# Kernel tuning notes

Measured on AMD Instinct MI355X. Metric: run time of the kernel, lower is better.

The kernel has to match this reference:

```python
import jax, jax.numpy as jnp
import numpy as np

N, SEQ_LEN, HORIZON, F_IN, EMBED, HIDDEN, LAYERS = 4096, 168, 24, 32, 32, 64, 2
G4 = 4 * HIDDEN
# NOTE: original torch code calls nn.LSTM per-step WITHOUT carrying hidden state,
# so each step's LSTM starts from (h0=0, c0=0): W_hh contributes nothing, only b_hh.

def setup_inputs() -> dict:
    key = jax.random.key(0)
    ks = jax.random.split(key, 12)
    s = 0.1
    return {
        "X": jax.random.normal(ks[0], (N, SEQ_LEN, F_IN), jnp.float32),
        "y": jax.random.normal(ks[1], (N, SEQ_LEN), jnp.float32),
        "Xf": jax.random.normal(ks[2], (N, HORIZON, F_IN), jnp.float32),
        "W_embed": jax.random.normal(ks[3], (EMBED, 1), jnp.float32) * s,
        "b_embed": jax.random.normal(ks[4], (EMBED,), jnp.float32) * s,
        "W_ih": jax.random.normal(ks[5], (LAYERS, G4, EMBED + F_IN), jnp.float32) * s,  # layer1 in-dim == HIDDEN == EMBED+F_IN
        "b_ih": jax.random.normal(ks[6], (LAYERS, G4), jnp.float32) * s,
        "b_hh": jax.random.normal(ks[7], (LAYERS, G4), jnp.float32) * s,
        "W_mu": jax.random.normal(ks[8], (1, HIDDEN), jnp.float32) * s,
        "b_mu": jax.random.normal(ks[9], (1,), jnp.float32) * s,
        "W_sigma": jax.random.normal(ks[10], (1, HIDDEN), jnp.float32) * s,
        "b_sigma": jax.random.normal(ks[11], (1,), jnp.float32) * s,
    }


def reference(X, y, Xf, W_embed, b_embed, W_ih, b_ih, b_hh, W_mu, b_mu, W_sigma, b_sigma):
    num_ts = X.shape[0]
    T = SEQ_LEN + HORIZON
    Xall = jnp.concatenate([X, Xf], axis=1)  # (N, T, F_IN)
    y_pad = jnp.concatenate([y, jnp.zeros((num_ts, HORIZON), y.dtype)], axis=1)  # (N, T)
    use_y = jnp.arange(T) < SEQ_LEN  # teacher-forced region

    def step(carry, inputs):
        x_s, y_s, use = inputs  # (N, F_IN), (N,), scalar bool
        ynext = jnp.where(use, y_s[:, None], carry)  # (N, 1)
        yembed = ynext @ W_embed.T + b_embed  # (N, EMBED)
        h = jnp.concatenate([x_s, yembed], axis=1)  # (N, F_IN+EMBED)
        for l in range(LAYERS):  # single LSTM step from zero state per layer
            gates = h @ W_ih[l].T + b_ih[l] + b_hh[l]  # (N, 4H); torch gate order i,f,g,o
            i_g, f_g, g_g, o_g = jnp.split(gates, 4, axis=1)
            c = jax.nn.sigmoid(i_g) * jnp.tanh(g_g)  # f * c0 term vanishes (c0 = 0)
            h = jax.nn.sigmoid(o_g) * jnp.tanh(c)
        h = jax.nn.relu(h)
        mu = h @ W_mu.T + b_mu  # (N, 1)
        sigma = jax.nn.softplus(h @ W_sigma.T + b_sigma) + 1e-6  # log(1+exp(.)) + eps
        lik = (2.0 * np.pi * sigma ** 2) ** (-0.5) * jnp.exp(-((ynext - mu) ** 2) / (2.0 * sigma ** 2))
        return lik, (lik[:, 0], mu[:, 0], sigma[:, 0])

    carry0 = jnp.zeros((num_ts, 1), X.dtype)
    xs = (jnp.swapaxes(Xall, 0, 1), y_pad.T, use_y)
    _, (lik_t, mu_t, sigma_t) = jax.lax.scan(step, carry0, xs)  # each (T, N)
    ypred = lik_t.T[:, SEQ_LEN - 1: SEQ_LEN + HORIZON - 1]  # (N, HORIZON)
    return ypred, mu_t.T, sigma_t.T
```

## Files before the change

### kernel.cpp

```cpp
#include <hip/hip_runtime.h>
#include <math.h>

#define N_TS 4096
#define SEQ  168
#define HOR  24
#define T_ALL 192
#define F_INP 32
#define HID  64
#define NROW 192
#define NB_B (N_TS / 16)
#define NT_B ((N_TS * SEQ) / 64)
#define L2E  1.44269504089f
#define W16F_L1  6144
#define W16F_L1P 18432

typedef _Float16 half8  __attribute__((ext_vector_type(8)));
typedef _Float16 half4  __attribute__((ext_vector_type(4)));
typedef float    floatx4 __attribute__((ext_vector_type(4)));

__device__ __forceinline__ float fexp(float x)  { return __expf(x); }
__device__ __forceinline__ float ex2(float x)   { return __builtin_amdgcn_exp2f(x); }
__device__ __forceinline__ float frcp(float x)  { return __builtin_amdgcn_rcpf(x); }
__device__ __forceinline__ float softplus_(float x) { return (x > 15.0f) ? x : __logf(1.0f + fexp(x)); }

__device__ __forceinline__ float lstm_h(float ip, float gp, float op) {
    const float Ei = ex2(ip);
    const float Eg = ex2(gp);
    const float cc = (1.0f - Eg) * frcp((1.0f + Ei) * (1.0f + Eg));
    const float Ec = ex2(cc * (-2.0f * L2E));
    const float Eo = ex2(op);
    return (1.0f - Ec) * frcp((1.0f + Ec) * (1.0f + Eo));
}

__device__ __forceinline__ half8 cvt8(const float4 a, const float4 b) {
    half8 v;
    v[0]=(_Float16)a.x; v[1]=(_Float16)a.y; v[2]=(_Float16)a.z; v[3]=(_Float16)a.w;
    v[4]=(_Float16)b.x; v[5]=(_Float16)b.y; v[6]=(_Float16)b.z; v[7]=(_Float16)b.w;
    return v;
}

__global__ __launch_bounds__(256) void prep(
    const float* __restrict__ W_ih, const float* __restrict__ b_ih,
    const float* __restrict__ b_hh,
    const float* __restrict__ W_embed, const float* __restrict__ b_embed,
    _Float16* __restrict__ W16f, float* __restrict__ bsum,
    float* __restrict__ wy1, float* __restrict__ b1c)
{
    const int idx = blockIdx.x * 256 + threadIdx.x;
    for (int i = idx; i < 4 * NROW * 8; i += gridDim.x * 256) {
        const int kp  = i & 7;
        const int row = (i >> 3) % NROW;
        const int kb  = (i >> 3) / NROW;
        const int sr  = (row < 64) ? row : row + 64;
        const float sc = (row >= 64 && row < 128) ? (-2.0f * L2E) : (-L2E);
        W16f[i] = (_Float16)(W_ih[sr * HID + kb * 8 + kp] * sc);
    }
    for (int i = idx; i < 8 * NROW * 8; i += gridDim.x * 256) {
        const int kp  = i & 7;
        const int row = (i >> 3) % NROW;
        const int kb  = (i >> 3) / NROW;
        const int sr  = (row < 64) ? row : row + 64;
        const float sc = (row >= 64 && row < 128) ? (-2.0f * L2E) : (-L2E);
        W16f[W16F_L1 + i] = (_Float16)(W_ih[(256 + sr) * HID + kb * 8 + kp] * sc);
    }
    for (int i = idx; i < 8 * NROW * 8; i += gridDim.x * 256) {
        const int kp  = i & 7;
        const int row = (i >> 3) % NROW;
        const int kb  = (i >> 3) / NROW;
        const int k   = kb * 8 + kp;
        const int kk  = k & 31;
        const int d   = (kk >> 1) & 3;
        const int q   = kk >> 3;
        const int e   = kk & 1;
        const int hid = d * 16 + q * 4 + ((k >> 5) << 1) + e;
        const int sr  = (row < 64) ? row : row + 64;
        const float sc = (row >= 64 && row < 128) ? (-2.0f * L2E) : (-L2E);
        W16f[W16F_L1P + i] = (_Float16)(W_ih[(256 + sr) * HID + hid] * sc);
    }
    for (int i = idx; i < 2 * NROW; i += gridDim.x * 256) {
        const int r = i % NROW;
        const int l = i / NROW;
        const int sr = (r < 64) ? r : r + 64;
        const float sc = (r >= 64 && r < 128) ? (-2.0f * L2E) : (-L2E);
        bsum[i] = (b_ih[l * 256 + sr] + b_hh[l * 256 + sr]) * sc;
    }
    if (idx < NROW) {
        const int sr = (idx < 64) ? idx : idx + 64;
        const float sc = (idx >= 64 && idx < 128) ? (-2.0f * L2E) : (-L2E);
        const float* wrow = W_ih + sr * HID + 32;
        float s1 = 0.f, s2 = 0.f;
        #pragma unroll
        for (int k = 0; k < 32; ++k) {
            s1 = fmaf(wrow[k], W_embed[k], s1);
            s2 = fmaf(wrow[k], b_embed[k], s2);
        }
        wy1[idx] = s1 * sc;
        b1c[idx] = (b_ih[sr] + b_hh[sr] + s2) * sc;
    }
}

__global__ __launch_bounds__(256, 6) void fused(
    const float* __restrict__ X,
    const float* __restrict__ y,
    const float* __restrict__ Xf,
    const float* __restrict__ W_embed,
    const float* __restrict__ b_embed,
    const _Float16* __restrict__ W16f,
    const float* __restrict__ bsum,
    const float* __restrict__ wy1,
    const float* __restrict__ b1c,
    const float* __restrict__ W_mu,
    const float* __restrict__ b_mu,
    const float* __restrict__ W_sigma,
    const float* __restrict__ b_sigma,
    float* __restrict__ out)
{
    __shared__ struct __align__(16) {
        _Float16 slab[16 * 64]; float partm[16][4]; float parts[16][4];
        float wyb[NROW]; float b1cb[NROW];
    } sh;

    const int tid = threadIdx.x;
    float* mu_out = out + (size_t)N_TS * HOR;
    float* sg_out = mu_out + (size_t)N_TS * T_ALL;

    if (blockIdx.x < NB_B) {
        __builtin_amdgcn_s_setprio(1);
        const int w    = tid >> 6;
        const int lane = tid & 63;
        const int quad = lane >> 4;
        const int ln   = lane & 15;
        const int n0   = blockIdx.x * 16;

        if (tid < NROW) {
            sh.wyb[tid]  = wy1[tid];
            sh.b1cb[tid] = b1c[tid];
        }

        half8 B1[3];
        half8 B2[3][2];
        float bias2[3];
        #pragma unroll
        for (int j = 0; j < 3; ++j) {
            const int rt = j * 4 + w;
            B1[j] = *(const half8*)(W16f + ((size_t)quad * NROW + rt * 16 + ln) * 8);
            #pragma unroll
            for (int kt = 0; kt < 2; ++kt)
                B2[j][kt] = *(const half8*)(W16f + W16F_L1 + ((size_t)(kt * 4 + quad) * NROW + rt * 16 + ln) * 8);
            bias2[j] = bsum[NROW + rt * 16 + ln];
        }
        const float wmu = W_mu[w * 16 + ln], wsg = W_sigma[w * 16 + ln];
        const float bmu = b_mu[0], bsg = b_sigma[0];

        const float* xfp = Xf + (size_t)(n0 + ln) * HOR * F_INP + quad * 8;
        float4 xa, xb;
        {
            const float* xp = X + ((size_t)(n0 + ln) * SEQ + (SEQ - 1)) * F_INP + quad * 8;
            xa = *(const float4*)xp;
            xb = *(const float4*)(xp + 4);
        }
        float ycur = y[(size_t)(n0 + ln) * SEQ + (SEQ - 1)];
        __syncthreads();

        #pragma unroll 1
        for (int it = 0; it <= HOR + 1; ++it) {
            if (it > 0) {
                const int k = it - 1;
                const float4 m4 = *(const float4*)sh.partm[ln];
                const float4 s4 = *(const float4*)sh.parts[ln];
                const float mu = (m4.x + m4.y) + (m4.z + m4.w) + bmu;
                const float sg = softplus_((s4.x + s4.y) + (s4.z + s4.w) + bsg) + 1e-6f;
                const float d  = ycur - mu;
                const float is = frcp(sg);
                const float lik = 0.39894228040143267f * is * fexp(-0.5f * d * d * is * is);
                if (k > 0 && w == 0 && quad == 0) {
                    const int nn = n0 + ln;
                    const int t  = SEQ + k - 1;
                    mu_out[(size_t)nn * T_ALL + t] = mu;
                    sg_out[(size_t)nn * T_ALL + t] = sg;
                    if (k < HOR) out[(size_t)nn * HOR + k] = lik;
                }
                ycur = lik;
            }
            if (it > HOR) break;

            const half8 xf0 = cvt8(xa, xb);
            if (it < HOR) {
                xa = *(const float4*)(xfp + it * F_INP);
                xb = *(const float4*)(xfp + it * F_INP + 4);
            }

            floatx4 t0 = *(const floatx4*)(sh.b1cb + 0 * 64 + w * 16 + quad * 4);
            floatx4 t1 = *(const floatx4*)(sh.b1cb + 1 * 64 + w * 16 + quad * 4);
            floatx4 t2 = *(const floatx4*)(sh.b1cb + 2 * 64 + w * 16 + quad * 4);
            t0 = __builtin_amdgcn_mfma_f32_16x16x32_f16(B1[0], xf0, t0, 0, 0, 0);
            t1 = __builtin_amdgcn_mfma_f32_16x16x32_f16(B1[1], xf0, t1, 0, 0, 0);
            t2 = __builtin_amdgcn_mfma_f32_16x16x32_f16(B1[2], xf0, t2, 0, 0, 0);

            const floatx4 wy0  = *(const floatx4*)(sh.wyb + 0 * 64 + w * 16 + quad * 4);
            const floatx4 wy1v = *(const floatx4*)(sh.wyb + 1 * 64 + w * 16 + quad * 4);
            const floatx4 wy2  = *(const floatx4*)(sh.wyb + 2 * 64 + w * 16 + quad * 4);

            half4 h1p;
            #pragma unroll
            for (int r = 0; r < 4; ++r) {
                const float ig = fmaf(ycur, wy0[r],  t0[r]);
                const float gg = fmaf(ycur, wy1v[r], t1[r]);
                const float og = fmaf(ycur, wy2[r],  t2[r]);
                h1p[r] = (_Float16)lstm_h(ig, gg, og);
            }
            {
                const int xblk = (2 * w + (quad >> 1)) ^ (ln & 7);
                *(half4*)(&sh.slab[ln * 64 + xblk * 8 + (quad & 1) * 4]) = h1p;
            }
            __syncthreads();

            const half8 a0 = *(const half8*)(&sh.slab[ln * 64 + ((quad ^ (ln & 7)) << 3)]);
            const half8 a1 = *(const half8*)(&sh.slab[ln * 64 + (((4 + quad) ^ (ln & 7)) << 3)]);
            floatx4 acc[3];
            #pragma unroll
            for (int j = 0; j < 3; ++j) {
                acc[j] = (floatx4){bias2[j], bias2[j], bias2[j], bias2[j]};
                acc[j] = __builtin_amdgcn_mfma_f32_16x16x32_f16(a0, B2[j][0], acc[j], 0, 0, 0);
                acc[j] = __builtin_amdgcn_mfma_f32_16x16x32_f16(a1, B2[j][1], acc[j], 0, 0, 0);
            }

            float pmr[4], psr[4];
            #pragma unroll
            for (int r = 0; r < 4; ++r) {
                const float hh = lstm_h(acc[0][r], acc[1][r], acc[2][r]);
                const float hr = fmaxf(hh, 0.0f);
                pmr[r] = hr * wmu;
                psr[r] = hr * wsg;
            }
            #pragma unroll
            for (int off = 1; off < 16; off <<= 1) {
                #pragma unroll
                for (int r = 0; r < 4; ++r) {
                    pmr[r] += __shfl_xor(pmr[r], off, 64);
                    psr[r] += __shfl_xor(psr[r], off, 64);
                }
            }
            if (ln == 0) {
                #pragma unroll
                for (int r = 0; r < 4; ++r) {
                    sh.partm[quad * 4 + r][w] = pmr[r];
                    sh.parts[quad * 4 + r][w] = psr[r];
                }
            }
            __syncthreads();
        }
        return;
    }

    const int w    = tid >> 6;
    const int lane = tid & 63;
    const int quad = lane >> 4;
    const int ln   = lane & 15;
    const int cid  = (blockIdx.x - NB_B) * 64 + w * 16 + ln;

    half8 xfr;
    {
        const float* xp = X + (size_t)cid * F_INP + quad * 8;
        xfr = cvt8(*(const float4*)xp, *(const float4*)(xp + 4));
    }
    const float yv = y[cid];

    half8 a0, a1;
    {
        const _Float16* bp = W16f + quad * 1536 + ln * 8;
        #pragma unroll
        for (int jt = 0; jt < 4; ++jt) {
            floatx4 ai = *(const floatx4*)(b1c + jt * 16 + quad * 4);
            floatx4 ag = *(const floatx4*)(b1c + 64 + jt * 16 + quad * 4);
            floatx4 ao = *(const floatx4*)(b1c + 128 + jt * 16 + quad * 4);
            ai = __builtin_amdgcn_mfma_f32_16x16x32_f16(*(const half8*)(bp + jt * 128),        xfr, ai, 0, 0, 0);
            ag = __builtin_amdgcn_mfma_f32_16x16x32_f16(*(const half8*)(bp + 512 + jt * 128),  xfr, ag, 0, 0, 0);
            ao = __builtin_amdgcn_mfma_f32_16x16x32_f16(*(const half8*)(bp + 1024 + jt * 128), xfr, ao, 0, 0, 0);
            const floatx4 wyi = *(const floatx4*)(wy1 + jt * 16 + quad * 4);
            const floatx4 wyg = *(const floatx4*)(wy1 + 64 + jt * 16 + quad * 4);
            const floatx4 wyo = *(const floatx4*)(wy1 + 128 + jt * 16 + quad * 4);
            a0[2 * jt + 0] = (_Float16)lstm_h(fmaf(yv, wyi[0], ai[0]),
                                              fmaf(yv, wyg[0], ag[0]),
                                              fmaf(yv, wyo[0], ao[0]));
            a0[2 * jt + 1] = (_Float16)lstm_h(fmaf(yv, wyi[1], ai[1]),
                                              fmaf(yv, wyg[1], ag[1]),
                                              fmaf(yv, wyo[1], ao[1]));
            a1[2 * jt + 0] = (_Float16)lstm_h(fmaf(yv, wyi[2], ai[2]),
                                              fmaf(yv, wyg[2], ag[2]),
                                              fmaf(yv, wyo[2], ao[2]));
            a1[2 * jt + 1] = (_Float16)lstm_h(fmaf(yv, wyi[3], ai[3]),
                                              fmaf(yv, wyg[3], ag[3]),
                                              fmaf(yv, wyo[3], ao[3]));
        }
    }

    float pm = 0.f, ps = 0.f;
    {
        const _Float16* bp = W16f + W16F_L1P + quad * 1536 + ln * 8;
        #pragma unroll
        for (int jt = 0; jt < 4; ++jt) {
            floatx4 ai = *(const floatx4*)(bsum + NROW + jt * 16 + quad * 4);
            floatx4 ag = *(const floatx4*)(bsum + NROW + 64 + jt * 16 + quad * 4);
            floatx4 ao = *(const floatx4*)(bsum + NROW + 128 + jt * 16 + quad * 4);
            ai = __builtin_amdgcn_mfma_f32_16x16x32_f16(*(const half8*)(bp + jt * 128),               a0, ai, 0, 0, 0);
            ai = __builtin_amdgcn_mfma_f32_16x16x32_f16(*(const half8*)(bp + 6144 + jt * 128),        a1, ai, 0, 0, 0);
            ag = __builtin_amdgcn_mfma_f32_16x16x32_f16(*(const half8*)(bp + 512 + jt * 128),         a0, ag, 0, 0, 0);
            ag = __builtin_amdgcn_mfma_f32_16x16x32_f16(*(const half8*)(bp + 6144 + 512 + jt * 128),  a1, ag, 0, 0, 0);
            ao = __builtin_amdgcn_mfma_f32_16x16x32_f16(*(const half8*)(bp + 1024 + jt * 128),        a0, ao, 0, 0, 0);
            ao = __builtin_amdgcn_mfma_f32_16x16x32_f16(*(const half8*)(bp + 6144 + 1024 + jt * 128), a1, ao, 0, 0, 0);
            const floatx4 wm  = *(const floatx4*)(W_mu + jt * 16 + quad * 4);
            const floatx4 ws4 = *(const floatx4*)(W_sigma + jt * 16 + quad * 4);
            #pragma unroll
            for (int r = 0; r < 4; ++r) {
                const float hr = fmaxf(lstm_h(ai[r], ag[r], ao[r]), 0.0f);
                pm = fmaf(hr, wm[r], pm);
                ps = fmaf(hr, ws4[r], ps);
            }
        }
    }
    pm += __shfl_xor(pm, 16, 64); pm += __shfl_xor(pm, 32, 64);
    ps += __shfl_xor(ps, 16, 64); ps += __shfl_xor(ps, 32, 64);

    if (quad == 0) {
        const int n = cid / SEQ;
        const int t = cid - n * SEQ;
        const float mu = pm + b_mu[0];
        const float sg = softplus_(ps + b_sigma[0]) + 1e-6f;
        mu_out[(size_t)n * T_ALL + t] = mu;
        sg_out[(size_t)n * T_ALL + t] = sg;
        if (t == SEQ - 1) {
            const float d  = yv - mu;
            const float is = frcp(sg);
            out[(size_t)n * HOR] = 0.39894228040143267f * is * fexp(-0.5f * d * d * is * is);
        }
    }
}

extern "C" void kernel_launch(void* const* d_in, const int* in_sizes, int n_in,
                              void* d_out, int out_size, void* d_ws, size_t ws_size,
                              hipStream_t stream) {
    const float* X       = (const float*)d_in[0];
    const float* y       = (const float*)d_in[1];
    const float* Xf      = (const float*)d_in[2];
    const float* W_embed = (const float*)d_in[3];
    const float* b_embed = (const float*)d_in[4];
    const float* W_ih    = (const float*)d_in[5];
    const float* b_ih    = (const float*)d_in[6];
    const float* b_hh    = (const float*)d_in[7];
    const float* W_mu    = (const float*)d_in[8];
    const float* b_mu    = (const float*)d_in[9];
    const float* W_sigma = (const float*)d_in[10];
    const float* b_sigma = (const float*)d_in[11];

    float* out = (float*)d_out;
    _Float16*  W16f = (_Float16*)d_ws;
    float*     bsum = (float*)((char*)d_ws + 61440);
    float*     wy1  = (float*)((char*)d_ws + 61440 + 1536);
    float*     b1c  = (float*)((char*)d_ws + 61440 + 1536 + 768);

    prep<<<96, 256, 0, stream>>>(W_ih, b_ih, b_hh, W_embed, b_embed,
                                 W16f, bsum, wy1, b1c);

    fused<<<NB_B + NT_B, 256, 0, stream>>>(
        X, y, Xf, W_embed, b_embed, W16f, bsum, wy1, b1c,
        W_mu, b_mu, W_sigma, b_sigma, out);
}
```

Measured before the change: 275.8 us.

## Use persistent teacher-forced blocks with atomic work queue and LDS-staged weights

The teacher-forced part switches from one short block per 64 timesteps to a fixed pool of 1024 persistent 512-thread blocks. Each block stages the layer weights, biases and head weights into shared memory once, then pulls 16-row units from a global atomic counter. The autoregressive blocks now handle 32 series each, as two 16-series groups in one 512-thread block. This cuts block launch overhead and repeated global weight loads, and balances work dynamically against the long-running recurrent blocks. In exchange it adds one atomic per unit and a counter that the prep kernel must reset, and the larger shared-memory union may lower occupancy.

Result: slower. 1.012 ms (+267.1%).

```diff
diff --git a/kernel.cpp b/kernel.cpp
--- a/kernel.cpp
+++ b/kernel.cpp
@@ -8,8 +8,9 @@
 #define F_INP 32
 #define HID  64
 #define NROW 192
-#define NB_B (N_TS / 16)
-#define NT_B ((N_TS * SEQ) / 64)
+#define NB_B (N_TS / 32)
+#define NT_B 1024
+#define NU   ((N_TS * SEQ) / 16)
 #define L2E  1.44269504089f
 #define W16F_L1  6144
 #define W16F_L1P 18432
@@ -44,9 +45,11 @@
     const float* __restrict__ b_hh,
     const float* __restrict__ W_embed, const float* __restrict__ b_embed,
     _Float16* __restrict__ W16f, float* __restrict__ bsum,
-    float* __restrict__ wy1, float* __restrict__ b1c)
+    float* __restrict__ wy1, float* __restrict__ b1c,
+    int* __restrict__ unit_cnt)
 {
     const int idx = blockIdx.x * 256 + threadIdx.x;
+    if (idx == 0) *unit_cnt = 0;
     for (int i = idx; i < 4 * NROW * 8; i += gridDim.x * 256) {
         const int kp  = i & 7;
         const int row = (i >> 3) % NROW;
@@ -99,7 +102,7 @@
     }
 }
 
-__global__ __launch_bounds__(256, 6) void fused(
+__global__ __launch_bounds__(512, 6) void fused(
     const float* __restrict__ X,
     const float* __restrict__ y,
     const float* __restrict__ Xf,
@@ -113,11 +116,21 @@
     const float* __restrict__ b_mu,
     const float* __restrict__ W_sigma,
     const float* __restrict__ b_sigma,
+    int* __restrict__ unit_cnt,
     float* __restrict__ out)
 {
-    __shared__ struct __align__(16) {
-        _Float16 slab[16 * 64]; float partm[16][4]; float parts[16][4];
-        float wyb[NROW]; float b1cb[NROW];
+    __shared__ union __align__(16) {
+        struct {
+            _Float16 Wl0[6144];
+            _Float16 Wl1[12288];
+            float b1cb[NROW]; float wy1b[NROW]; float bs1b[NROW];
+            float wmb[HID]; float wsb[HID];
+        } P;
+        struct {
+            _Float16 slab[2][1024];
+            float partm[2][16][4]; float parts[2][16][4];
+            float wyb[NROW]; float b1cb[NROW];
+        } B;
     } sh;
 
     const int tid = threadIdx.x;
@@ -127,14 +140,16 @@
     if (blockIdx.x < NB_B) {
         __builtin_amdgcn_s_setprio(1);
         const int w    = tid >> 6;
+        const int g    = w >> 2;
+        const int wg   = w & 3;
         const int lane = tid & 63;
         const int quad = lane >> 4;
         const int ln   = lane & 15;
-        const int n0   = blockIdx.x * 16;
+        const int n0   = blockIdx.x * 32 + g * 16;
 
         if (tid < NROW) {
-            sh.wyb[tid]  = wy1[tid];
-            sh.b1cb[tid] = b1c[tid];
+            sh.B.wyb[tid]  = wy1[tid];
+            sh.B.b1cb[tid] = b1c[tid];
         }
 
         half8 B1[3];
@@ -142,14 +157,14 @@
         float bias2[3];
         #pragma unroll
         for (int j = 0; j < 3; ++j) {
-            const int rt = j * 4 + w;
+            const int rt = j * 4 + wg;
             B1[j] = *(const half8*)(W16f + ((size_t)quad * NROW + rt * 16 + ln) * 8);
             #pragma unroll
             for (int kt = 0; kt < 2; ++kt)
                 B2[j][kt] = *(const half8*)(W16f + W16F_L1 + ((size_t)(kt * 4 + quad) * NROW + rt * 16 + ln) * 8);
             bias2[j] = bsum[NROW + rt * 16 + ln];
         }
-        const float wmu = W_mu[w * 16 + ln], wsg = W_sigma[w * 16 + ln];
+        const float wmu = W_mu[wg * 16 + ln], wsg = W_sigma[wg * 16 + ln];
         const float bmu = b_mu[0], bsg = b_sigma[0];
 
         const float* xfp = Xf + (size_t)(n0 + ln) * HOR * F_INP + quad * 8;
@@ -166,14 +181,14 @@
         for (int it = 0; it <= HOR + 1; ++it) {
             if (it > 0) {
                 const int k = it - 1;
-                const float4 m4 = *(const float4*)sh.partm[ln];
-                const float4 s4 = *(const float4*)sh.parts[ln];
+                const float4 m4 = *(const float4*)sh.B.partm[g][ln];
+                const float4 s4 = *(const float4*)sh.B.parts[g][ln];
                 const float mu = (m4.x + m4.y) + (m4.z + m4.w) + bmu;
                 const float sg = softplus_((s4.x + s4.y) + (s4.z + s4.w) + bsg) + 1e-6f;
                 const float d  = ycur - mu;
                 const float is = frcp(sg);
                 const float lik = 0.39894228040143267f * is * fexp(-0.5f * d * d * is * is);
-                if (k > 0 && w == 0 && quad == 0) {
+                if (k > 0 && wg == 0 && quad == 0) {
                     const int nn = n0 + ln;
                     const int t  = SEQ + k - 1;
                     mu_out[(size_t)nn * T_ALL + t] = mu;
@@ -190,16 +205,16 @@
                 xb = *(const float4*)(xfp + it * F_INP + 4);
             }
 
-            floatx4 t0 = *(const floatx4*)(sh.b1cb + 0 * 64 + w * 16 + quad * 4);
-            floatx4 t1 = *(const floatx4*)(sh.b1cb + 1 * 64 + w * 16 + quad * 4);
-            floatx4 t2 = *(const floatx4*)(sh.b1cb + 2 * 64 + w * 16 + quad * 4);
+            floatx4 t0 = *(const floatx4*)(sh.B.b1cb + 0 * 64 + wg * 16 + quad * 4);
+            floatx4 t1 = *(const floatx4*)(sh.B.b1cb + 1 * 64 + wg * 16 + quad * 4);
+            floatx4 t2 = *(const floatx4*)(sh.B.b1cb + 2 * 64 + wg * 16 + quad * 4);
             t0 = __builtin_amdgcn_mfma_f32_16x16x32_f16(B1[0], xf0, t0, 0, 0, 0);
             t1 = __builtin_amdgcn_mfma_f32_16x16x32_f16(B1[1], xf0, t1, 0, 0, 0);
             t2 = __builtin_amdgcn_mfma_f32_16x16x32_f16(B1[2], xf0, t2, 0, 0, 0);
 
-            const floatx4 wy0  = *(const floatx4*)(sh.wyb + 0 * 64 + w * 16 + quad * 4);
-            const floatx4 wy1v = *(const floatx4*)(sh.wyb + 1 * 64 + w * 16 + quad * 4);
-            const floatx4 wy2  = *(const floatx4*)(sh.wyb + 2 * 64 + w * 16 + quad * 4);
+            const floatx4 wy0  = *(const floatx4*)(sh.B.wyb + 0 * 64 + wg * 16 + quad * 4);
+            const floatx4 wy1v = *(const floatx4*)(sh.B.wyb + 1 * 64 + wg * 16 + quad * 4);
+            const floatx4 wy2  = *(const floatx4*)(sh.B.wyb + 2 * 64 + wg * 16 + quad * 4);
 
             half4 h1p;
             #pragma unroll
@@ -210,13 +225,13 @@
                 h1p[r] = (_Float16)lstm_h(ig, gg, og);
             }
             {
-                const int xblk = (2 * w + (quad >> 1)) ^ (ln & 7);
-                *(half4*)(&sh.slab[ln * 64 + xblk * 8 + (quad & 1) * 4]) = h1p;
+                const int xblk = (2 * wg + (quad >> 1)) ^ (ln & 7);
+                *(half4*)(&sh.B.slab[g][ln * 64 + xblk * 8 + (quad & 1) * 4]) = h1p;
             }
             __syncthreads();
 
-            const half8 a0 = *(const half8*)(&sh.slab[ln * 64 + ((quad ^ (ln & 7)) << 3)]);
-            const half8 a1 = *(const half8*)(&sh.slab[ln * 64 + (((4 + quad) ^ (ln & 7)) << 3)]);
+            const half8 a0 = *(const half8*)(&sh.B.slab[g][ln * 64 + ((quad ^ (ln & 7)) << 3)]);
+            const half8 a1 = *(const half8*)(&sh.B.slab[g][ln * 64 + (((4 + quad) ^ (ln & 7)) << 3)]);
             floatx4 acc[3];
             #pragma unroll
             for (int j = 0; j < 3; ++j) {
@@ -244,8 +259,8 @@
             if (ln == 0) {
                 #pragma unroll
                 for (int r = 0; r < 4; ++r) {
-                    sh.partm[quad * 4 + r][w] = pmr[r];
-                    sh.parts[quad * 4 + r][w] = psr[r];
+                    sh.B.partm[g][quad * 4 + r][wg] = pmr[r];
+                    sh.B.parts[g][quad * 4 + r][wg] = psr[r];
                 }
             }
             __syncthreads();
@@ -253,33 +268,53 @@
         return;
     }
 
-    const int w    = tid >> 6;
     const int lane = tid & 63;
     const int quad = lane >> 4;
     const int ln   = lane & 15;
-    const int cid  = (blockIdx.x - NB_B) * 64 + w * 16 + ln;
-
-    half8 xfr;
-    {
+
+    for (int i = tid; i < 768; i += 512)
+        *(half8*)(sh.P.Wl0 + i * 8) = *(const half8*)(W16f + i * 8);
+    for (int i = tid; i < 1536; i += 512)
+        *(half8*)(sh.P.Wl1 + i * 8) = *(const half8*)(W16f + W16F_L1P + i * 8);
+    if (tid < NROW) {
+        sh.P.b1cb[tid] = b1c[tid];
+        sh.P.wy1b[tid] = wy1[tid];
+        sh.P.bs1b[tid] = bsum[NROW + tid];
+    }
+    if (tid < HID) { sh.P.wmb[tid] = W_mu[tid]; sh.P.wsb[tid] = W_sigma[tid]; }
+    __syncthreads();
+
+    const _Float16* bp0 = sh.P.Wl0 + quad * 1536 + ln * 8;
+    const _Float16* bp1 = sh.P.Wl1 + quad * 1536 + ln * 8;
+    const float bmu = b_mu[0], bsg = b_sigma[0];
+
+    int u0 = 0;
+    if (lane == 0) u0 = atomicAdd(unit_cnt, 1);
+    int u = __builtin_amdgcn_readfirstlane(u0);
+
+    while (u < NU) {
+        int unext = 0;
+        if (lane == 0) unext = atomicAdd(unit_cnt, 1);
+
+        const int cid = u * 16 + ln;
         const float* xp = X + (size_t)cid * F_INP + quad * 8;
-        xfr = cvt8(*(const float4*)xp, *(const float4*)(xp + 4));
-    }
-    const float yv = y[cid];
-
-    half8 a0, a1;
-    {
-        const _Float16* bp = W16f + quad * 1536 + ln * 8;
+        const float4 x0v = *(const float4*)xp;
+        const float4 x1v = *(const float4*)(xp + 4);
+        const float yv = y[cid];
+        const half8 xfr = cvt8(x0v, x1v);
+
+        half8 a0, a1;
         #pragma unroll
         for (int jt = 0; jt < 4; ++jt) {
-            floatx4 ai = *(const floatx4*)(b1c + jt * 16 + quad * 4);
-            floatx4 ag = *(const floatx4*)(b1c + 64 + jt * 16 + quad * 4);
-            floatx4 ao = *(const floatx4*)(b1c + 128 + jt * 16 + quad * 4);
-            ai = __builtin_amdgcn_mfma_f32_16x16x32_f16(*(const half8*)(bp + jt * 128),        xfr, ai, 0, 0, 0);
-            ag = __builtin_amdgcn_mfma_f32_16x16x32_f16(*(const half8*)(bp + 512 + jt * 128),  xfr, ag, 0, 0, 0);
-            ao = __builtin_amdgcn_mfma_f32_16x16x32_f16(*(const half8*)(bp + 1024 + jt * 128), xfr, ao, 0, 0, 0);
-            const floatx4 wyi = *(const floatx4*)(wy1 + jt * 16 + quad * 4);
-            const floatx4 wyg = *(const floatx4*)(wy1 + 64 + jt * 16 + quad * 4);
-            const floatx4 wyo = *(const floatx4*)(wy1 + 128 + jt * 16 + quad * 4);
+            floatx4 ai = *(const floatx4*)(sh.P.b1cb + jt * 16 + quad * 4);
+            floatx4 ag = *(const floatx4*)(sh.P.b1cb + 64 + jt * 16 + quad * 4);
+            floatx4 ao = *(const floatx4*)(sh.P.b1cb + 128 + jt * 16 + quad * 4);
+            ai = __builtin_amdgcn_mfma_f32_16x16x32_f16(*(const half8*)(bp0 + jt * 128),        xfr, ai, 0, 0, 0);
+            ag = __builtin_amdgcn_mfma_f32_16x16x32_f16(*(const half8*)(bp0 + 512 + jt * 128),  xfr, ag, 0, 0, 0);
+            ao = __builtin_amdgcn_mfma_f32_16x16x32_f16(*(const half8*)(bp0 + 1024 + jt * 128), xfr, ao, 0, 0, 0);
+            const floatx4 wyi = *(const floatx4*)(sh.P.wy1b + jt * 16 + quad * 4);
+            const floatx4 wyg = *(const floatx4*)(sh.P.wy1b + 64 + jt * 16 + quad * 4);
+            const floatx4 wyo = *(const floatx4*)(sh.P.wy1b + 128 + jt * 16 + quad * 4);
             a0[2 * jt + 0] = (_Float16)lstm_h(fmaf(yv, wyi[0], ai[0]),
                                               fmaf(yv, wyg[0], ag[0]),
                                               fmaf(yv, wyo[0], ao[0]));
@@ -293,24 +328,21 @@
                                               fmaf(yv, wyg[3], ag[3]),
                                               fmaf(yv, wyo[3], ao[3]));
         }
-    }
-
-    float pm = 0.f, ps = 0.f;
-    {
-        const _Float16* bp = W16f + W16F_L1P + quad * 1536 + ln * 8;
+
+        float pm = 0.f, ps = 0.f;
         #pragma unroll
         for (int jt = 0; jt < 4; ++jt) {
-            floatx4 ai = *(const floatx4*)(bsum + NROW + jt * 16 + quad * 4);
-            floatx4 ag = *(const floatx4*)(bsum + NROW + 64 + jt * 16 + quad * 4);
-            floatx4 ao = *(const floatx4*)(bsum + NROW + 128 + jt * 16 + quad * 4);
-            ai = __builtin_amdgcn_mfma_f32_16x16x32_f16(*(const half8*)(bp + jt * 128),               a0, ai, 0, 0, 0);
-            ai = __builtin_amdgcn_mfma_f32_16x16x32_f16(*(const half8*)(bp + 6144 + jt * 128),        a1, ai, 0, 0, 0);
-            ag = __builtin_amdgcn_mfma_f32_16x16x32_f16(*(const half8*)(bp + 512 + jt * 128),         a0, ag, 0, 0, 0);
-            ag = __builtin_amdgcn_mfma_f32_16x16x32_f16(*(const half8*)(bp + 6144 + 512 + jt * 128),  a1, ag, 0, 0, 0);
-            ao = __builtin_amdgcn_mfma_f32_16x16x32_f16(*(const half8*)(bp + 1024 + jt * 128),        a0, ao, 0, 0, 0);
-            ao = __builtin_amdgcn_mfma_f32_16x16x32_f16(*(const half8*)(bp + 6144 + 1024 + jt * 128), a1, ao, 0, 0, 0);
-            const floatx4 wm  = *(const floatx4*)(W_mu + jt * 16 + quad * 4);
-            const floatx4 ws4 = *(const floatx4*)(W_sigma + jt * 16 + quad * 4);
+            floatx4 ai = *(const floatx4*)(sh.P.bs1b + jt * 16 + quad * 4);
+            floatx4 ag = *(const floatx4*)(sh.P.bs1b + 64 + jt * 16 + quad * 4);
+            floatx4 ao = *(const floatx4*)(sh.P.bs1b + 128 + jt * 16 + quad * 4);
+            ai = __builtin_amdgcn_mfma_f32_16x16x32_f16(*(const half8*)(bp1 + jt * 128),               a0, ai, 0, 0, 0);
+            ai = __builtin_amdgcn_mfma_f32_16x16x32_f16(*(const half8*)(bp1 + 6144 + jt * 128),        a1, ai, 0, 0, 0);
+            ag = __builtin_amdgcn_mfma_f32_16x16x32_f16(*(const half8*)(bp1 + 512 + jt * 128),         a0, ag, 0, 0, 0);
+            ag = __builtin_amdgcn_mfma_f32_16x16x32_f16(*(const half8*)(bp1 + 6144 + 512 + jt * 128),  a1, ag, 0, 0, 0);
+            ao = __builtin_amdgcn_mfma_f32_16x16x32_f16(*(const half8*)(bp1 + 1024 + jt * 128),        a0, ao, 0, 0, 0);
+            ao = __builtin_amdgcn_mfma_f32_16x16x32_f16(*(const half8*)(bp1 + 6144 + 1024 + jt * 128), a1, ao, 0, 0, 0);
+            const floatx4 wm  = *(const floatx4*)(sh.P.wmb + jt * 16 + quad * 4);
+            const floatx4 ws4 = *(const floatx4*)(sh.P.wsb + jt * 16 + quad * 4);
             #pragma unroll
             for (int r = 0; r < 4; ++r) {
                 const float hr = fmaxf(lstm_h(ai[r], ag[r], ao[r]), 0.0f);
@@ -318,22 +350,23 @@
                 ps = fmaf(hr, ws4[r], ps);
             }
         }
-    }
-    pm += __shfl_xor(pm, 16, 64); pm += __shfl_xor(pm, 32, 64);
-    ps += __shfl_xor(ps, 16, 64); ps += __shfl_xor(ps, 32, 64);
-
-    if (quad == 0) {
-        const int n = cid / SEQ;
-        const int t = cid - n * SEQ;
-        const float mu = pm + b_mu[0];
-        const float sg = softplus_(ps + b_sigma[0]) + 1e-6f;
-        mu_out[(size_t)n * T_ALL + t] = mu;
-        sg_out[(size_t)n * T_ALL + t] = sg;
-        if (t == SEQ - 1) {
-            const float d  = yv - mu;
-            const float is = frcp(sg);
-            out[(size_t)n * HOR] = 0.39894228040143267f * is * fexp(-0.5f * d * d * is * is);
-        }
+        pm += __shfl_xor(pm, 16, 64); pm += __shfl_xor(pm, 32, 64);
+        ps += __shfl_xor(ps, 16, 64); ps += __shfl_xor(ps, 32, 64);
+
+        if (quad == 0) {
+            const int n = cid / SEQ;
+            const int t = cid - n * SEQ;
+            const float mu = pm + bmu;
+            const float sg = softplus_(ps + bsg) + 1e-6f;
+            mu_out[(size_t)n * T_ALL + t] = mu;
+            sg_out[(size_t)n * T_ALL + t] = sg;
+            if (t == SEQ - 1) {
+                const float d  = yv - mu;
+                const float is = frcp(sg);
+                out[(size_t)n * HOR] = 0.39894228040143267f * is * fexp(-0.5f * d * d * is * is);
+            }
+        }
+        u = __builtin_amdgcn_readfirstlane(unext);
     }
 }
 
@@ -354,15 +387,16 @@
     const float* b_sigma = (const float*)d_in[11];
 
     float* out = (float*)d_out;
-    _Float16*  W16f = (_Float16*)d_ws;
-    float*     bsum = (float*)((char*)d_ws + 61440);
-    float*     wy1  = (float*)((char*)d_ws + 61440 + 1536);
-    float*     b1c  = (float*)((char*)d_ws + 61440 + 1536 + 768);
+    _Float16*  W16f     = (_Float16*)d_ws;
+    float*     bsum     = (float*)((char*)d_ws + 61440);
+    float*     wy1      = (float*)((char*)d_ws + 61440 + 1536);
+    float*     b1c      = (float*)((char*)d_ws + 61440 + 1536 + 768);
+    int*       unit_cnt = (int*)((char*)d_ws + 61440 + 1536 + 768 + 768);
 
     prep<<<96, 256, 0, stream>>>(W_ih, b_ih, b_hh, W_embed, b_embed,
-                                 W16f, bsum, wy1, b1c);
-
-    fused<<<NB_B + NT_B, 256, 0, stream>>>(
+                                 W16f, bsum, wy1, b1c, unit_cnt);
+
+    fused<<<NB_B + NT_B, 512, 0, stream>>>(
         X, y, Xf, W_embed, b_embed, W16f, bsum, wy1, b1c,
-        W_mu, b_mu, W_sigma, b_sigma, out);
+        W_mu, b_mu, W_sigma, b_sigma, unit_cnt, out);
 }
```
